# Kernel optimization log

Hardware: AMD Instinct MI355X
Metric: run time of the kernel (lower is better)

The kernel has to match this reference:

```python
import jax, jax.numpy as jnp
import numpy as np

B0, C0, H0, W0 = 32, 512, 64, 64  # x shape; L = C0 = d_model
DC = 32   # c_increase (per-direction inner dim)
NS = 16   # d_state
RK = 32   # dt_rank = ceil(512/16)


def setup_inputs() -> dict:
    key = jax.random.key(0)
    ks = jax.random.split(key, 8)
    x = jax.random.normal(ks[0], (B0, C0, H0, W0), jnp.float32)
    xc_proj_weight = jax.random.normal(ks[1], (2, RK + 2 * NS, DC), jnp.float32) * 0.05
    dtc_projs_weight = jax.random.uniform(ks[2], (2, DC, RK), jnp.float32, -RK ** -0.5, RK ** -0.5)
    # inv-softplus of dt sampled log-uniform in [1e-3, 1e-1]
    dt = jnp.exp(jax.random.uniform(ks[3], (2, DC)) * (np.log(0.1) - np.log(0.001)) + np.log(0.001))
    dtc_projs_bias = dt + jnp.log(-jnp.expm1(-dt))
    Ac_logs = jnp.log(jnp.tile(jnp.arange(1, NS + 1, dtype=jnp.float32), (2 * DC, 1)))  # [2D, N]
    Dcs = jnp.ones((2 * DC,), jnp.float32)
    w_cin = jax.random.normal(ks[4], (DC, 2), jnp.float32) * 0.5    # Conv2d(2, DC, 1) weight
    bn_gamma = jnp.ones((DC,), jnp.float32)
    bn_beta = jnp.zeros((DC,), jnp.float32)
    bn_mean = jnp.zeros((DC,), jnp.float32)
    bn_var = jnp.ones((DC,), jnp.float32)
    w_cout = jax.random.normal(ks[5], (DC,), jnp.float32) * 0.2     # Conv2d(DC, 1, 1) weight
    ln_gamma = jnp.ones((C0,), jnp.float32)
    ln_beta = jnp.zeros((C0,), jnp.float32)
    return dict(x=x, xc_proj_weight=xc_proj_weight, dtc_projs_weight=dtc_projs_weight,
                dtc_projs_bias=dtc_projs_bias, Ac_logs=Ac_logs, Dcs=Dcs, w_cin=w_cin,
                bn_gamma=bn_gamma, bn_beta=bn_beta, bn_mean=bn_mean, bn_var=bn_var,
                w_cout=w_cout, ln_gamma=ln_gamma, ln_beta=ln_beta)


def _selective_scan(u, delta, A, Bs, Cs, D, delta_bias):
    # u, delta: [B, 2D, L]; A: [2D, N]; Bs, Cs: [B, 2, N, L] (K=2 groups); D, delta_bias: [2D]
    B, KD, L = u.shape
    d_per = KD // Bs.shape[1]
    delta = jax.nn.softplus(delta + delta_bias[None, :, None])
    Bg = jnp.repeat(Bs, d_per, axis=1)  # [B, 2D, N, L] (group = d // d_per)
    Cg = jnp.repeat(Cs, d_per, axis=1)
    dA = jnp.exp(delta[:, :, None, :] * A[None, :, :, None])      # [B, 2D, N, L]
    dBu = delta[:, :, None, :] * Bg * u[:, :, None, :]            # [B, 2D, N, L]

    def step(h, inp):
        dA_l, dBu_l = inp
        h = dA_l * h + dBu_l
        return h, h

    h0 = jnp.zeros((B, KD, dA.shape[2]), u.dtype)
    _, hs = jax.lax.scan(step, h0, (jnp.moveaxis(dA, 3, 0), jnp.moveaxis(dBu, 3, 0)))  # [L, B, 2D, N]
    y = jnp.einsum('lbdn,bdnl->bdl', hs, Cg) + D[None, :, None] * u
    return y


def reference(x, xc_proj_weight, dtc_projs_weight, dtc_projs_bias, Ac_logs, Dcs,
              w_cin, bn_gamma, bn_beta, bn_mean, bn_var, w_cout, ln_gamma, ln_beta):
    B, C, H, W = x.shape
    L = C
    avg = jnp.mean(x, axis=(2, 3))          # [B, C]
    mx = jnp.max(x, axis=(2, 3))            # [B, C]
    xsc = jnp.stack([avg, mx], axis=1)       # [B, 2, C]
    # 1x1 conv (2 -> DC) over 'spatial' dim C, + BatchNorm(eval) + GELU
    h = jnp.einsum('bic,di->bdc', xsc, w_cin)  # [B, DC, L]
    h = (h - bn_mean[None, :, None]) * jax.lax.rsqrt(bn_var + 1e-5)[None, :, None]
    h = h * bn_gamma[None, :, None] + bn_beta[None, :, None]
    h = jax.nn.gelu(h, approximate=False)
    # bidirectional stacking
    xk = jnp.stack([h, jnp.flip(h, axis=-1)], axis=1)  # [B, 2, DC, L]
    dbl = jnp.einsum('bkdl,kcd->bkcl', xk, xc_proj_weight)  # [B, 2, R+2N, L]
    dts, Bs, Cs = dbl[:, :, :RK], dbl[:, :, RK:RK + NS], dbl[:, :, RK + NS:]
    dts = jnp.einsum('bkrl,kdr->bkdl', dts, dtc_projs_weight)  # [B, 2, DC, L]
    u = xk.reshape(B, 2 * DC, L)
    delta = dts.reshape(B, 2 * DC, L)
    A = -jnp.exp(Ac_logs)  # [2D, N]
    out_y = _selective_scan(u, delta, A, Bs, Cs, Dcs, dtc_projs_bias.reshape(-1))
    out_y = out_y.reshape(B, 2, DC, L)
    y = out_y[:, 0] + jnp.flip(out_y[:, 1], axis=-1)  # [B, DC, L]
    # 1x1 conv (DC -> 1, no bias) + GELU
    y = jax.nn.gelu(jnp.einsum('bdl,d->bl', y, w_cout), approximate=False)  # [B, L]
    # LayerNorm over channel dim (d_model = C)
    mu = jnp.mean(y, axis=-1, keepdims=True)
    var = jnp.var(y, axis=-1, keepdims=True)
    attn = (y - mu) * jax.lax.rsqrt(var + 1e-5) * ln_gamma[None, :] + ln_beta[None, :]
    attn = attn[:, :, None, None]  # [B, C, 1, 1]
    return x + x * attn
```

## Files before the change

### kernel.cpp

```cpp
#include <hip/hip_runtime.h>
#include <math.h>

#define B0 32
#define C0 512
#define HW 4096
#define DC 32
#define NS 16
#define RK 32
#define L  512
#define KD 64
#define CB 64
#define NCH (L / CB)
#define NBK 64
#define FSTR 16

#define LOAD_ACQ(p)    __hip_atomic_load((p), __ATOMIC_ACQUIRE, __HIP_MEMORY_SCOPE_AGENT)
#define LOAD_RLX(p)    __hip_atomic_load((p), __ATOMIC_RELAXED, __HIP_MEMORY_SCOPE_AGENT)
#define STORE_RLX(p,v) __hip_atomic_store((p), (v), __ATOMIC_RELAXED, __HIP_MEMORY_SCOPE_AGENT)
#define STORE_REL(p,v) __hip_atomic_store((p), (v), __ATOMIC_RELEASE, __HIP_MEMORY_SCOPE_AGENT)

__device__ __forceinline__ float gelu_exact(float x) {
    return 0.5f * x * (1.0f + erff(x * 0.70710678118654752f));
}
__device__ __forceinline__ float softplus_f(float x) {
    float ax = fabsf(x);
    return fmaxf(x, 0.0f) + log1pf(expf(-ax));
}

__global__ __launch_bounds__(256) void pool_kernel(const float* __restrict__ x,
                                                   float* __restrict__ avg,
                                                   float* __restrict__ mx,
                                                   int* __restrict__ flags) {
    int row = blockIdx.x;
    if (row < NBK * NCH && threadIdx.x == 0) flags[row * FSTR] = 0;
    const float4* xr = (const float4*)(x + (size_t)row * HW);
    int tid = threadIdx.x;
    float s = 0.f, m = -INFINITY;
#pragma unroll
    for (int i = 0; i < 4; ++i) {
        float4 v = xr[tid + i * 256];
        s += v.x + v.y + v.z + v.w;
        m = fmaxf(m, fmaxf(fmaxf(v.x, v.y), fmaxf(v.z, v.w)));
    }
    for (int off = 32; off > 0; off >>= 1) {
        s += __shfl_down(s, off, 64);
        m = fmaxf(m, __shfl_down(m, off, 64));
    }
    __shared__ float ss[4], sm[4];
    int wave = tid >> 6;
    if ((tid & 63) == 0) { ss[wave] = s; sm[wave] = m; }
    __syncthreads();
    if (tid == 0) {
        s = ss[0] + ss[1] + ss[2] + ss[3];
        m = fmaxf(fmaxf(sm[0], sm[1]), fmaxf(sm[2], sm[3]));
        avg[row] = s * (1.0f / HW);
        mx[row] = m;
    }
}

__global__ __launch_bounds__(512) void mid_kernel(
    const float* __restrict__ avg, const float* __restrict__ mx,
    const float* __restrict__ w_cin,
    const float* __restrict__ bn_g, const float* __restrict__ bn_b,
    const float* __restrict__ bn_m, const float* __restrict__ bn_v,
    const float* __restrict__ xcw, const float* __restrict__ dtw,
    const float* __restrict__ dtb,
    const float* __restrict__ Ac_logs, const float* __restrict__ Dcs,
    const float* __restrict__ w_cout,
    float* __restrict__ hendg,
    float* __restrict__ sdeg,
    int* __restrict__ flags,
    float* __restrict__ ybl2)
{
    __shared__ float sW[64 * DC];
    __shared__ float sPW[DC * RK];
    __shared__ float sh_c[DC * (CB + 1)];
    __shared__ float sde[DC * (CB + 1)];
    __shared__ float sdtred[DC * (CB + 1)];
    __shared__ float sB[CB * (NS + 1)];
    __shared__ float sC[CB * (NS + 1)];

    float* sdt = sdtred;
    float* red = sdtred;

    int bk = blockIdx.x & (NBK - 1);
    int c  = blockIdx.x >> 6;
    int k = bk & 1;
    int b = bk >> 1;
    int base = bk * NCH;
    int lidx = base + c;
    int tid = threadIdx.x;

    for (int i = tid; i < 64 * DC; i += 512) sW[i]  = xcw[k * 64 * DC + i];
    for (int i = tid; i < DC * RK; i += 512) sPW[i] = dtw[k * DC * RK + i];

    int l0 = k ? (L - (c + 1) * CB) : c * CB;

    for (int i = tid; i < DC * CB; i += 512) {
        int d = i >> 6, ll = i & (CB - 1);
        int gl = l0 + ll;
        float a = avg[b * C0 + gl], m = mx[b * C0 + gl];
        float v = a * w_cin[d * 2] + m * w_cin[d * 2 + 1];
        v = (v - bn_m[d]) * rsqrtf(bn_v[d] + 1e-5f);
        v = v * bn_g[d] + bn_b[d];
        sh_c[d * (CB + 1) + ll] = gelu_exact(v);
    }
    __syncthreads();

    for (int idx = tid; idx < 64 * CB; idx += 512) {
        int cc = idx >> 6, ll = idx & (CB - 1);
        float acc = 0.f;
#pragma unroll
        for (int d = 0; d < DC; ++d) acc += sh_c[d * (CB + 1) + ll] * sW[cc * DC + d];
        if (cc < RK) sdt[cc * CB + ll] = acc;
        else if (cc < RK + NS) sB[ll * (NS + 1) + (cc - RK)] = acc;
        else sC[ll * (NS + 1) + (cc - RK - NS)] = acc;
    }
    __syncthreads();

    for (int idx = tid; idx < DC * CB; idx += 512) {
        int d = idx >> 6, ll = idx & (CB - 1);
        float acc = dtb[k * DC + d];
#pragma unroll
        for (int r = 0; r < RK; ++r) acc += sdt[r * CB + ll] * sPW[d * RK + r];
        sde[d * (CB + 1) + ll] = softplus_f(acc);
    }
    __syncthreads();

    int d_s = tid >> 4;
    int n_s = tid & 15;
    int kd  = k * DC + d_s;
    float A = -expf(Ac_logs[kd * NS + n_s]);
    float hloc = 0.f, sdsum = 0.f;
#pragma unroll 4
    for (int sl = 0; sl < CB; ++sl) {
        int ll = k ? (CB - 1 - sl) : sl;
        float de = sde[d_s * (CB + 1) + ll];
        float u  = sh_c[d_s * (CB + 1) + ll];
        float Bv = sB[ll * (NS + 1) + n_s];
        hloc = expf(de * A) * hloc + de * Bv * u;
        sdsum += de;
    }

    if (c < NCH - 1) {
        STORE_RLX(hendg + (size_t)lidx * (DC * NS) + tid, hloc);
        if (n_s == 0) STORE_RLX(sdeg + lidx * DC + d_s, sdsum);
        __syncthreads();
        if (tid == 0) STORE_REL(flags + lidx * FSTR, 1);
    }

    float cin = 0.f;
    if (c > 0) {
        if (tid < c) {
            const int* fp = flags + (base + tid) * FSTR;
            while (LOAD_ACQ(fp) == 0) __builtin_amdgcn_s_sleep(2);
        }
        __syncthreads();
        for (int j = 0; j < c; ++j) {
            float sd = LOAD_RLX(sdeg + (base + j) * DC + d_s);
            float he = LOAD_RLX(hendg + (size_t)(base + j) * (DC * NS) + tid);
            cin = expf(A * sd) * cin + he;
        }
    }

    float w  = w_cout[d_s];
    float Dv = Dcs[kd];
    float hs = cin;
#pragma unroll 4
    for (int sl = 0; sl < CB; ++sl) {
        int ll = k ? (CB - 1 - sl) : sl;
        float de = sde[d_s * (CB + 1) + ll];
        float u  = sh_c[d_s * (CB + 1) + ll];
        float Bv = sB[ll * (NS + 1) + n_s];
        float Cv = sC[ll * (NS + 1) + n_s];
        hs = expf(de * A) * hs + de * Bv * u;
        float contrib = hs * Cv;
        contrib += __shfl_xor(contrib, 1, 16);
        contrib += __shfl_xor(contrib, 2, 16);
        contrib += __shfl_xor(contrib, 4, 16);
        contrib += __shfl_xor(contrib, 8, 16);
        if (n_s == 0) red[d_s * (CB + 1) + ll] = w * (contrib + Dv * u);
    }
    __syncthreads();

    if (tid < CB) {
        int ll = tid;
        float acc = 0.f;
#pragma unroll
        for (int dd = 0; dd < DC; ++dd) acc += red[dd * (CB + 1) + ll];
        ybl2[(size_t)bk * L + l0 + ll] = acc;
    }
}

__global__ __launch_bounds__(512) void epi_kernel(const float* __restrict__ ybl2,
                                                  const float* __restrict__ ln_g,
                                                  const float* __restrict__ ln_b,
                                                  float* __restrict__ attn) {
    int b = blockIdx.x;
    int l = threadIdx.x;
    float y = gelu_exact(ybl2[(size_t)(b * 2) * L + l] + ybl2[(size_t)(b * 2 + 1) * L + l]);
    float s = y, s2 = y * y;
    for (int off = 32; off > 0; off >>= 1) {
        s += __shfl_down(s, off, 64);
        s2 += __shfl_down(s2, off, 64);
    }
    __shared__ float ss[8], ss2[8];
    __shared__ float smu, srv;
    int wave = l >> 6;
    if ((l & 63) == 0) { ss[wave] = s; ss2[wave] = s2; }
    __syncthreads();
    if (l == 0) {
        float ts = 0.f, ts2 = 0.f;
#pragma unroll
        for (int i = 0; i < 8; ++i) { ts += ss[i]; ts2 += ss2[i]; }
        float mu = ts * (1.0f / L);
        float var = ts2 * (1.0f / L) - mu * mu;
        smu = mu;
        srv = rsqrtf(var + 1e-5f);
    }
    __syncthreads();
    attn[b * C0 + l] = (y - smu) * srv * ln_g[l] + ln_b[l];
}

__global__ __launch_bounds__(256) void gate_kernel(const float* __restrict__ x,
                                                   const float* __restrict__ attn,
                                                   float* __restrict__ out) {
    const float4* x4 = (const float4*)x;
    float4* o4 = (float4*)out;
    size_t base = (size_t)blockIdx.x * 2048 + threadIdx.x;
#pragma unroll
    for (int i = 0; i < 8; ++i) {
        size_t t = base + (size_t)i * 256;
        float4 v = x4[t];
        float a = 1.0f + attn[t >> 10];
        v.x *= a; v.y *= a; v.z *= a; v.w *= a;
        o4[t] = v;
    }
}

extern "C" void kernel_launch(void* const* d_in, const int* in_sizes, int n_in,
                              void* d_out, int out_size, void* d_ws, size_t ws_size,
                              hipStream_t stream) {
    const float* x     = (const float*)d_in[0];
    const float* xcw   = (const float*)d_in[1];
    const float* dtw   = (const float*)d_in[2];
    const float* dtb   = (const float*)d_in[3];
    const float* Aclog = (const float*)d_in[4];
    const float* Dcs   = (const float*)d_in[5];
    const float* wcin  = (const float*)d_in[6];
    const float* bng   = (const float*)d_in[7];
    const float* bnb   = (const float*)d_in[8];
    const float* bnm   = (const float*)d_in[9];
    const float* bnv   = (const float*)d_in[10];
    const float* wcout = (const float*)d_in[11];
    const float* lng   = (const float*)d_in[12];
    const float* lnb   = (const float*)d_in[13];
    float* out = (float*)d_out;

    float* ws = (float*)d_ws;
    float* avg   = ws;
    float* mx    = ws + 16384;
    float* ybl2  = ws + 32768;
    float* attn  = ws + 65536;
    float* hendg = ws + 81920;
    float* sdeg  = ws + 344064;
    int*   flags = (int*)(ws + 360448);

    pool_kernel<<<B0 * C0, 256, 0, stream>>>(x, avg, mx, flags);
    mid_kernel<<<NBK * NCH, 512, 0, stream>>>(avg, mx, wcin, bng, bnb, bnm, bnv,
                                              xcw, dtw, dtb, Aclog, Dcs, wcout,
                                              hendg, sdeg, flags, ybl2);
    epi_kernel<<<B0, 512, 0, stream>>>(ybl2, lng, lnb, attn);
    gate_kernel<<<(B0 * C0 * HW / 4) / 2048, 256, 0, stream>>>(x, attn, out);
}
```

Before: 553.1 us.

## Fuse LayerNorm epilogue into scan kernel via last-block counter; reverse gate order

Removes the separate epilogue launch. Each scan block atomically increments a per-batch counter, and the last block to finish for a batch computes GELU, the LayerNorm and attn. The gate kernel now walks chunks in reverse so it touches first the x data most recently read by the pool kernel, which may still be in cache, and it writes the output with nontemporal stores. In exchange this adds atomic traffic and an extra counter reset in the pool kernel.

```diff
diff --git a/kernel.cpp b/kernel.cpp
--- a/kernel.cpp
+++ b/kernel.cpp
@@ -19,6 +19,8 @@
 #define STORE_RLX(p,v) __hip_atomic_store((p), (v), __ATOMIC_RELAXED, __HIP_MEMORY_SCOPE_AGENT)
 #define STORE_REL(p,v) __hip_atomic_store((p), (v), __ATOMIC_RELEASE, __HIP_MEMORY_SCOPE_AGENT)
 
+typedef float f32x4 __attribute__((ext_vector_type(4)));
+
 __device__ __forceinline__ float gelu_exact(float x) {
     return 0.5f * x * (1.0f + erff(x * 0.70710678118654752f));
 }
@@ -30,9 +32,11 @@
 __global__ __launch_bounds__(256) void pool_kernel(const float* __restrict__ x,
                                                    float* __restrict__ avg,
                                                    float* __restrict__ mx,
-                                                   int* __restrict__ flags) {
+                                                   int* __restrict__ flags,
+                                                   int* __restrict__ cnt) {
     int row = blockIdx.x;
     if (row < NBK * NCH && threadIdx.x == 0) flags[row * FSTR] = 0;
+    if (row < B0 && threadIdx.x == 64) cnt[row] = 0;
     const float4* xr = (const float4*)(x + (size_t)row * HW);
     int tid = threadIdx.x;
     float s = 0.f, m = -INFINITY;
@@ -67,10 +71,13 @@
     const float* __restrict__ dtb,
     const float* __restrict__ Ac_logs, const float* __restrict__ Dcs,
     const float* __restrict__ w_cout,
+    const float* __restrict__ ln_g, const float* __restrict__ ln_b,
     float* __restrict__ hendg,
     float* __restrict__ sdeg,
     int* __restrict__ flags,
-    float* __restrict__ ybl2)
+    int* __restrict__ cnt,
+    float* __restrict__ ybl2,
+    float* __restrict__ attn)
 {
     __shared__ float sW[64 * DC];
     __shared__ float sPW[DC * RK];
@@ -188,53 +195,61 @@
         float acc = 0.f;
 #pragma unroll
         for (int dd = 0; dd < DC; ++dd) acc += red[dd * (CB + 1) + ll];
-        ybl2[(size_t)bk * L + l0 + ll] = acc;
-    }
-}
-
-__global__ __launch_bounds__(512) void epi_kernel(const float* __restrict__ ybl2,
-                                                  const float* __restrict__ ln_g,
-                                                  const float* __restrict__ ln_b,
-                                                  float* __restrict__ attn) {
-    int b = blockIdx.x;
-    int l = threadIdx.x;
-    float y = gelu_exact(ybl2[(size_t)(b * 2) * L + l] + ybl2[(size_t)(b * 2 + 1) * L + l]);
-    float s = y, s2 = y * y;
-    for (int off = 32; off > 0; off >>= 1) {
-        s += __shfl_down(s, off, 64);
-        s2 += __shfl_down(s2, off, 64);
-    }
-    __shared__ float ss[8], ss2[8];
-    __shared__ float smu, srv;
-    int wave = l >> 6;
-    if ((l & 63) == 0) { ss[wave] = s; ss2[wave] = s2; }
-    __syncthreads();
-    if (l == 0) {
-        float ts = 0.f, ts2 = 0.f;
-#pragma unroll
-        for (int i = 0; i < 8; ++i) { ts += ss[i]; ts2 += ss2[i]; }
-        float mu = ts * (1.0f / L);
-        float var = ts2 * (1.0f / L) - mu * mu;
-        smu = mu;
-        srv = rsqrtf(var + 1e-5f);
-    }
-    __syncthreads();
-    attn[b * C0 + l] = (y - smu) * srv * ln_g[l] + ln_b[l];
+        STORE_RLX(ybl2 + (size_t)bk * L + l0 + ll, acc);
+    }
+    __syncthreads();
+
+    __shared__ int isLast;
+    if (tid == 0) {
+        int old = __hip_atomic_fetch_add(&cnt[b], 1, __ATOMIC_ACQ_REL,
+                                         __HIP_MEMORY_SCOPE_AGENT);
+        isLast = (old == 2 * NCH - 1);
+    }
+    __syncthreads();
+    if (isLast) {
+        int l = tid;
+        float y0 = LOAD_RLX(ybl2 + (size_t)(b * 2) * L + l);
+        float y1 = LOAD_RLX(ybl2 + (size_t)(b * 2 + 1) * L + l);
+        float y = gelu_exact(y0 + y1);
+        float s = y, s2 = y * y;
+        for (int off = 32; off > 0; off >>= 1) {
+            s += __shfl_down(s, off, 64);
+            s2 += __shfl_down(s2, off, 64);
+        }
+        __shared__ float ss[8], ss2[8];
+        __shared__ float smu, srv;
+        int wave = l >> 6;
+        if ((l & 63) == 0) { ss[wave] = s; ss2[wave] = s2; }
+        __syncthreads();
+        if (l == 0) {
+            float ts = 0.f, ts2 = 0.f;
+#pragma unroll
+            for (int i = 0; i < 8; ++i) { ts += ss[i]; ts2 += ss2[i]; }
+            float mu = ts * (1.0f / L);
+            float var = ts2 * (1.0f / L) - mu * mu;
+            smu = mu;
+            srv = rsqrtf(var + 1e-5f);
+        }
+        __syncthreads();
+        attn[b * C0 + l] = (y - smu) * srv * ln_g[l] + ln_b[l];
+    }
 }
 
 __global__ __launch_bounds__(256) void gate_kernel(const float* __restrict__ x,
                                                    const float* __restrict__ attn,
                                                    float* __restrict__ out) {
-    const float4* x4 = (const float4*)x;
-    float4* o4 = (float4*)out;
-    size_t base = (size_t)blockIdx.x * 2048 + threadIdx.x;
+    const f32x4* x4 = (const f32x4*)x;
+    f32x4* o4 = (f32x4*)out;
+    int nblk = (int)gridDim.x;
+    int chunk = nblk - 1 - (int)blockIdx.x;
+    size_t base = (size_t)chunk * 2048 + threadIdx.x;
 #pragma unroll
     for (int i = 0; i < 8; ++i) {
         size_t t = base + (size_t)i * 256;
-        float4 v = x4[t];
+        f32x4 v = x4[t];
         float a = 1.0f + attn[t >> 10];
         v.x *= a; v.y *= a; v.z *= a; v.w *= a;
-        o4[t] = v;
+        __builtin_nontemporal_store(v, &o4[t]);
     }
 }
 
@@ -265,11 +280,12 @@
     float* hendg = ws + 81920;
     float* sdeg  = ws + 344064;
     int*   flags = (int*)(ws + 360448);
-
-    pool_kernel<<<B0 * C0, 256, 0, stream>>>(x, avg, mx, flags);
+    int*   cnt   = flags + NBK * NCH * FSTR;
+
+    pool_kernel<<<B0 * C0, 256, 0, stream>>>(x, avg, mx, flags, cnt);
     mid_kernel<<<NBK * NCH, 512, 0, stream>>>(avg, mx, wcin, bng, bnb, bnm, bnv,
                                               xcw, dtw, dtb, Aclog, Dcs, wcout,
-                                              hendg, sdeg, flags, ybl2);
-    epi_kernel<<<B0, 512, 0, stream>>>(ybl2, lng, lnb, attn);
+                                              lng, lnb, hendg, sdeg, flags, cnt,
+                                              ybl2, attn);
     gate_kernel<<<(B0 * C0 * HW / 4) / 2048, 256, 0, stream>>>(x, attn, out);
 }
```

Result: faster. 538.7 us (-2.6%).
